# Kernel optimization log

Measured on AMD Instinct MI355X. Metric: run time of the kernel, lower is better.

The kernel has to match this reference:

```python
import jax, jax.numpy as jnp
import numpy as np

HIDDEN = 30

def setup_inputs() -> dict:
    key = jax.random.key(0)
    ks = jax.random.split(key, 12)
    N, E, F, G, C = 100000, 1600000, 128, 2048, 2
    x = jax.random.normal(ks[0], (N, F), dtype=jnp.float32)
    edge_index = jax.random.randint(ks[1], (2, E), 0, N, dtype=jnp.int64)
    batch = jnp.sort(jax.random.randint(ks[2], (N,), 0, G, dtype=jnp.int64))
    def glorot(k, shape):
        lim = np.sqrt(6.0 / (shape[0] + shape[1]))
        return jax.random.uniform(k, shape, jnp.float32, -lim, lim)
    return {
        'x': x, 'edge_index': edge_index, 'batch': batch, 'num_graphs': G,
        'W0': glorot(ks[3], (F, HIDDEN)), 'b0': jnp.zeros((HIDDEN,), jnp.float32),
        'W1': glorot(ks[4], (HIDDEN, HIDDEN)), 'b1': jnp.zeros((HIDDEN,), jnp.float32),
        'W2': glorot(ks[5], (HIDDEN, HIDDEN)), 'b2': jnp.zeros((HIDDEN,), jnp.float32),
        'W3': glorot(ks[6], (HIDDEN, HIDDEN)), 'b3': jnp.zeros((HIDDEN,), jnp.float32),
        'Wlin': glorot(ks[7], (4 * HIDDEN, C)), 'blin': jnp.zeros((C,), jnp.float32),
    }


def _gcn_norm(edge_index, num_nodes):
    # Add self-loops, compute symmetric normalization (PyG GCNConv default).
    loops = jnp.arange(num_nodes, dtype=edge_index.dtype)
    row = jnp.concatenate([edge_index[0], loops])
    col = jnp.concatenate([edge_index[1], loops])
    deg = jax.ops.segment_sum(jnp.ones_like(col, dtype=jnp.float32), col,
                              num_segments=num_nodes)
    dis = jnp.where(deg > 0, jax.lax.rsqrt(deg), 0.0)
    norm = dis[row] * dis[col]  # [E + N]
    return row, col, norm


def _gcn_conv(x, W, b, row, col, norm, num_nodes):
    xw = x @ W                              # [N, H] transform first
    msg = xw[row] * norm[:, None]           # gather + scale  [E+N, H]
    out = jax.ops.segment_sum(msg, col, num_segments=num_nodes)  # scatter-add
    return out + b


def _max_pool(x, batch, num_graphs):
    out = jax.ops.segment_max(x, batch, num_segments=num_graphs)
    return jnp.where(jnp.isneginf(out), 0.0, out)


def reference(x, edge_index, batch, num_graphs, W0, b0, W1, b1, W2, b2, W3, b3, Wlin, blin):
    N = x.shape[0]
    row, col, norm = _gcn_norm(edge_index, N)
    outs = []
    h = jax.nn.relu(_gcn_conv(x, W0, b0, row, col, norm, N))
    outs.append(_max_pool(h, batch, num_graphs))
    h = jax.nn.relu(_gcn_conv(h, W1, b1, row, col, norm, N))
    outs.append(_max_pool(h, batch, num_graphs))
    h = jax.nn.relu(_gcn_conv(h, W2, b2, row, col, norm, N))
    outs.append(_max_pool(h, batch, num_graphs))
    h = _gcn_conv(h, W3, b3, row, col, norm, N)  # no ReLU on last conv
    outs.append(_max_pool(h, batch, num_graphs))
    readout = jnp.concatenate(outs, axis=-1)     # [G, 4*HIDDEN]
    return readout @ Wlin + blin                 # [G, num_classes]
```

## Files before the change

### kernel.cpp

```cpp
#include <hip/hip_runtime.h>
#include <math.h>

#define HIDDEN 30
#define SP 32


__global__ void k_hist(const int* __restrict__ col, unsigned* __restrict__ deg, int E) {
    int e = blockIdx.x * blockDim.x + threadIdx.x;
    if (e < E) atomicAdd(&deg[col[e]], 1u);
}

__global__ void k_dis(const unsigned* __restrict__ deg, float* __restrict__ dis, int N) {
    int i = blockIdx.x * blockDim.x + threadIdx.x;
    if (i < N) dis[i] = rsqrtf((float)deg[i] + 1.0f);
}

__global__ void k_scan_block(const unsigned* __restrict__ deg, unsigned* __restrict__ inc,
                             unsigned* __restrict__ bsum, int N) {
    __shared__ unsigned s[1024];
    int i = blockIdx.x * 1024 + threadIdx.x;
    unsigned v = (i < N) ? deg[i] : 0u;
    s[threadIdx.x] = v;
    __syncthreads();
    for (int off = 1; off < 1024; off <<= 1) {
        unsigned t = (threadIdx.x >= off) ? s[threadIdx.x - off] : 0u;
        __syncthreads();
        s[threadIdx.x] += t;
        __syncthreads();
    }
    if (i < N) inc[i] = s[threadIdx.x];
    if (threadIdx.x == 1023) bsum[blockIdx.x] = s[1023];
}

__global__ void k_scan_bsums(unsigned* __restrict__ bsum, int nb) {
    __shared__ unsigned s[128];
    int i = threadIdx.x;
    s[i] = (i < nb) ? bsum[i] : 0u;
    __syncthreads();
    for (int off = 1; off < 128; off <<= 1) {
        unsigned t = (i >= off) ? s[i - off] : 0u;
        __syncthreads();
        s[i] += t;
        __syncthreads();
    }
    if (i < nb) bsum[i] = s[i];
}

__global__ void k_rowptr(const unsigned* __restrict__ bsum, unsigned* __restrict__ rowptr, int N) {
    int i = blockIdx.x * 1024 + threadIdx.x;
    if (i >= N) return;
    int blk = i >> 10;
    if (blk) rowptr[i + 1] += bsum[blk - 1];
    if (i == 0) rowptr[0] = 0u;
}

__global__ void k_cnt_copy(const unsigned* __restrict__ rowptr, unsigned* __restrict__ cnt, int N) {
    int i = blockIdx.x * blockDim.x + threadIdx.x;
    if (i < N) cnt[i] = rowptr[i];
}

__global__ void k_scatter(const int* __restrict__ row, const int* __restrict__ col,
                          unsigned* __restrict__ cnt, int* __restrict__ src, int E) {
    int e = blockIdx.x * blockDim.x + threadIdx.x;
    if (e >= E) return;
    int c = col[e];
    unsigned p = atomicAdd(&cnt[c], 1u);
    src[p] = row[e];
}

__global__ void k_gstart(const int* __restrict__ batch, int* __restrict__ gstart, int N, int G) {
    int i = blockIdx.x * blockDim.x + threadIdx.x;
    if (i >= N) return;
    int b = batch[i];
    if (i == 0) {
        for (int g = 0; g <= b; ++g) gstart[g] = 0;
    } else {
        int p = batch[i - 1];
        if (p != b) for (int g = p + 1; g <= b; ++g) gstart[g] = i;
    }
    if (i == N - 1) {
        for (int g = b + 1; g <= G; ++g) gstart[g] = N;
    }
}


__global__ void k_transform0(const float* __restrict__ x, const float* __restrict__ W,
                             const float* __restrict__ dis, float* __restrict__ S, int N) {
    __shared__ float Ws[128 * HIDDEN];
    __shared__ float Xs[8 * 128];
    for (int i = threadIdx.x; i < 128 * HIDDEN; i += 256) Ws[i] = W[i];
    int nb = blockIdx.x * 8;
    for (int i = threadIdx.x; i < 8 * 128; i += 256) {
        int nn = nb + (i >> 7);
        Xs[i] = (nn < N) ? x[(size_t)nn * 128 + (i & 127)] : 0.f;
    }
    __syncthreads();
    int nl = threadIdx.x >> 5, h = threadIdx.x & 31;
    int n = nb + nl;
    if (n >= N) return;
    float acc = 0.f;
    if (h < HIDDEN) {
        const float* xr = &Xs[nl * 128];
#pragma unroll 8
        for (int f = 0; f < 128; ++f) acc += xr[f] * Ws[f * HIDDEN + h];
        acc *= dis[n];
    }
    S[(size_t)n * SP + h] = (h < HIDDEN) ? acc : 0.f;
}

__global__ void k_transform_small(const float* __restrict__ in, const float* __restrict__ W,
                                  const float* __restrict__ dis, float* __restrict__ S, int N) {
    __shared__ float Ws[HIDDEN * HIDDEN];
    __shared__ float Bs[8 * SP];
    for (int i = threadIdx.x; i < HIDDEN * HIDDEN; i += 256) Ws[i] = W[i];
    int nb = blockIdx.x * 8;
    {
        int i = threadIdx.x;
        int nn = nb + (i >> 5);
        Bs[i] = (nn < N) ? in[(size_t)nn * SP + (i & 31)] : 0.f;
    }
    __syncthreads();
    int nl = threadIdx.x >> 5, h = threadIdx.x & 31;
    int n = nb + nl;
    if (n >= N) return;
    float acc = 0.f;
    if (h < HIDDEN) {
        const float* r = &Bs[nl * SP];
#pragma unroll
        for (int k = 0; k < HIDDEN; ++k) acc += r[k] * Ws[k * HIDDEN + h];
        acc *= dis[n];
    }
    S[(size_t)n * SP + h] = (h < HIDDEN) ? acc : 0.f;
}

__global__ void k_agg(const unsigned* __restrict__ rowptr, const int* __restrict__ src,
                      const float4* __restrict__ S4, const float* __restrict__ dis,
                      const float* __restrict__ b, float4* __restrict__ B4, int N, int do_relu) {
    int w = threadIdx.x >> 6;
    int lane = threadIdx.x & 63;
    int n = blockIdx.x * 4 + w;
    if (n >= N) return;
    int g = lane >> 3, s = lane & 7;
    float ax = 0.f, ay = 0.f, az = 0.f, aw = 0.f;
    if (g == 0) {
        float4 v = S4[(size_t)n * 8 + s];
        ax = v.x; ay = v.y; az = v.z; aw = v.w;
    }
    unsigned beg = rowptr[n], end = rowptr[n + 1];
    for (unsigned j = beg + g; j < end; j += 8) {
        int r = src[j];
        float4 v = S4[(size_t)r * 8 + s];
        ax += v.x; ay += v.y; az += v.z; aw += v.w;
    }
    for (int off = 8; off < 64; off <<= 1) {
        ax += __shfl_xor(ax, off);
        ay += __shfl_xor(ay, off);
        az += __shfl_xor(az, off);
        aw += __shfl_xor(aw, off);
    }
    if (g == 0) {
        float d = dis[n];
        int h = s * 4;
        float o0 = (h + 0 < HIDDEN) ? d * ax + b[h + 0] : 0.f;
        float o1 = (h + 1 < HIDDEN) ? d * ay + b[h + 1] : 0.f;
        float o2 = (h + 2 < HIDDEN) ? d * az + b[h + 2] : 0.f;
        float o3 = (h + 3 < HIDDEN) ? d * aw + b[h + 3] : 0.f;
        if (do_relu) {
            o0 = fmaxf(o0, 0.f); o1 = fmaxf(o1, 0.f);
            o2 = fmaxf(o2, 0.f); o3 = fmaxf(o3, 0.f);
        }
        B4[(size_t)n * 8 + s] = make_float4(o0, o1, o2, o3);
    }
}

__global__ void k_pool(const float* __restrict__ B, const int* __restrict__ gstart,
                       float* __restrict__ pooled, int G) {
    int g = blockIdx.x * 4 + (threadIdx.x >> 6);
    if (g >= G) return;
    int lane = threadIdx.x & 63;
    int h = lane & 31;
    int sub = lane >> 5;
    int beg = gstart[g], end = gstart[g + 1];
    float m = -INFINITY;
    if (h < HIDDEN) {
        for (int i = beg + sub; i < end; i += 2) m = fmaxf(m, B[(size_t)i * SP + h]);
    }
    float o = __shfl_down(m, 32);
    m = fmaxf(m, o);
    if (sub == 0 && h < HIDDEN) pooled[(size_t)g * HIDDEN + h] = (end > beg) ? m : 0.0f;
}

__global__ void k_final(const float* __restrict__ pooled, const float* __restrict__ Wlin,
                        const float* __restrict__ blin, float* __restrict__ out, int G) {
    int g = blockIdx.x * blockDim.x + threadIdx.x;
    if (g >= G) return;
    float a0 = blin[0], a1 = blin[1];
#pragma unroll
    for (int l = 0; l < 4; ++l) {
        for (int h = 0; h < HIDDEN; ++h) {
            float v = pooled[((size_t)l * G + g) * HIDDEN + h];
            int k = l * HIDDEN + h;
            a0 += v * Wlin[k * 2 + 0];
            a1 += v * Wlin[k * 2 + 1];
        }
    }
    out[g * 2 + 0] = a0;
    out[g * 2 + 1] = a1;
}

static inline size_t align256(size_t x) { return (x + 255) & ~(size_t)255; }

extern "C" void kernel_launch(void* const* d_in, const int* in_sizes, int n_in,
                              void* d_out, int out_size, void* d_ws, size_t ws_size,
                              hipStream_t stream) {
    const float* x     = (const float*)d_in[0];
    const int*   ei    = (const int*)d_in[1];
    const int*   batch = (const int*)d_in[2];
    const float* W0 = (const float*)d_in[4];
    const float* b0 = (const float*)d_in[5];
    const float* W1 = (const float*)d_in[6];
    const float* b1 = (const float*)d_in[7];
    const float* W2 = (const float*)d_in[8];
    const float* b2 = (const float*)d_in[9];
    const float* W3 = (const float*)d_in[10];
    const float* b3 = (const float*)d_in[11];
    const float* Wlin = (const float*)d_in[12];
    const float* blin = (const float*)d_in[13];

    const int N = in_sizes[0] / 128;
    const int E = in_sizes[1] / 2;
    const int G = out_size / 2;
    const int* row = ei;
    const int* col = ei + E;

    char* ws = (char*)d_ws;
    size_t off = 0;
    unsigned* deg    = (unsigned*)(ws + off); off += align256((size_t)N * 4);
    unsigned* cnt    = (unsigned*)(ws + off); off += align256((size_t)N * 4);
    unsigned* rowptr = (unsigned*)(ws + off); off += align256(((size_t)N + 1) * 4);
    unsigned* bsum   = (unsigned*)(ws + off); off += align256(128 * 4);
    int*      gstart = (int*)(ws + off);      off += align256(((size_t)G + 1) * 4);
    float*    dis    = (float*)(ws + off);    off += align256((size_t)N * 4);
    int*      src    = (int*)(ws + off);      off += align256((size_t)E * 4);
    float*    S      = (float*)(ws + off);    off += align256((size_t)N * SP * 4);
    float*    B      = (float*)(ws + off);    off += align256((size_t)N * SP * 4);
    float*    pooled = (float*)(ws + off);    off += align256((size_t)4 * G * HIDDEN * 4);

    const float* Wl[4] = {W0, W1, W2, W3};
    const float* bl[4] = {b0, b1, b2, b3};

    hipMemsetAsync(deg, 0, (size_t)N * 4, stream);
    k_hist<<<(E + 255) / 256, 256, 0, stream>>>(col, deg, E);
    k_dis<<<(N + 255) / 256, 256, 0, stream>>>(deg, dis, N);
    int nb = (N + 1023) / 1024;
    k_scan_block<<<nb, 1024, 0, stream>>>(deg, rowptr + 1, bsum, N);
    k_scan_bsums<<<1, 128, 0, stream>>>(bsum, nb);
    k_rowptr<<<nb, 1024, 0, stream>>>(bsum, rowptr, N);
    k_cnt_copy<<<(N + 255) / 256, 256, 0, stream>>>(rowptr, cnt, N);
    k_scatter<<<(E + 255) / 256, 256, 0, stream>>>(row, col, cnt, src, E);
    k_gstart<<<(N + 255) / 256, 256, 0, stream>>>(batch, gstart, N, G);

    int nblk8 = (N + 7) / 8;
    int nblk4 = (N + 3) / 4;
    for (int l = 0; l < 4; ++l) {
        if (l == 0) k_transform0<<<nblk8, 256, 0, stream>>>(x, W0, dis, S, N);
        else        k_transform_small<<<nblk8, 256, 0, stream>>>(B, Wl[l], dis, S, N);
        k_agg<<<nblk4, 256, 0, stream>>>(rowptr, src, (const float4*)S, dis, bl[l],
                                         (float4*)B, N, l < 3 ? 1 : 0);
        k_pool<<<(G + 3) / 4, 256, 0, stream>>>(B, gstart, pooled + (size_t)l * G * HIDDEN, G);
    }

    k_final<<<(G + 255) / 256, 256, 0, stream>>>(pooled, Wlin, blin, (float*)d_out, G);
}
```

Measured before the change: 652.3 us.

## Replace random CSR scatter with two-pass bucketed radix partition

The single-pass atomic scatter of edges into CSR order is replaced by a coarse partition. Edges are first bucketed by destination-node range using per-block shared histograms, a single-block scan, and a bucketed pair scatter. A per-bucket pass then does the fine atomic placement, so global atomics and writes stay within a localized node range for better cache locality. The cost is extra passes, an 8-byte pair buffer per edge, and a serial single-block scan over 256x256 entries.

```diff
diff --git a/kernel.cpp b/kernel.cpp
--- a/kernel.cpp
+++ b/kernel.cpp
@@ -14,6 +14,7 @@
     int i = blockIdx.x * blockDim.x + threadIdx.x;
     if (i < N) dis[i] = rsqrtf((float)deg[i] + 1.0f);
 }
+
 
 __global__ void k_scan_block(const unsigned* __restrict__ deg, unsigned* __restrict__ inc,
                              unsigned* __restrict__ bsum, int N) {
@@ -59,13 +60,73 @@
     if (i < N) cnt[i] = rowptr[i];
 }
 
-__global__ void k_scatter(const int* __restrict__ row, const int* __restrict__ col,
-                          unsigned* __restrict__ cnt, int* __restrict__ src, int E) {
-    int e = blockIdx.x * blockDim.x + threadIdx.x;
-    if (e >= E) return;
-    int c = col[e];
-    unsigned p = atomicAdd(&cnt[c], 1u);
-    src[p] = row[e];
+
+__global__ void k_bhist(const int* __restrict__ col, unsigned* __restrict__ blockhist,
+                        int E, int chunk, int nblocks, int shift, int NB) {
+    __shared__ unsigned h[256];
+    for (int i = threadIdx.x; i < NB; i += 256) h[i] = 0;
+    __syncthreads();
+    int s = blockIdx.x * chunk, e = min(E, s + chunk);
+    for (int j = s + threadIdx.x; j < e; j += 256) atomicAdd(&h[col[j] >> shift], 1u);
+    __syncthreads();
+    for (int i = threadIdx.x; i < NB; i += 256)
+        blockhist[(size_t)i * nblocks + blockIdx.x] = h[i];
+}
+
+__global__ void k_bscan(unsigned* __restrict__ a, int M) {
+    __shared__ unsigned s[1024];
+    __shared__ unsigned carry;
+    if (threadIdx.x == 0) carry = 0;
+    __syncthreads();
+    for (int base = 0; base < M; base += 1024) {
+        int i = base + threadIdx.x;
+        unsigned v = (i < M) ? a[i] : 0u;
+        s[threadIdx.x] = v;
+        __syncthreads();
+        for (int off = 1; off < 1024; off <<= 1) {
+            unsigned t = (threadIdx.x >= off) ? s[threadIdx.x - off] : 0u;
+            __syncthreads();
+            s[threadIdx.x] += t;
+            __syncthreads();
+        }
+        unsigned excl = s[threadIdx.x] - v + carry;
+        if (i < M) a[i] = excl;
+        __syncthreads();
+        if (threadIdx.x == 1023) carry += s[1023];
+        __syncthreads();
+    }
+}
+
+__global__ void k_bscatter(const int* __restrict__ row, const int* __restrict__ col,
+                           const unsigned* __restrict__ bh, int2* __restrict__ pairs,
+                           int E, int chunk, int nblocks, int shift, int NB) {
+    __shared__ unsigned base[256];
+    __shared__ unsigned cnt[256];
+    for (int i = threadIdx.x; i < NB; i += 256) {
+        base[i] = bh[(size_t)i * nblocks + blockIdx.x];
+        cnt[i] = 0;
+    }
+    __syncthreads();
+    int s = blockIdx.x * chunk, e = min(E, s + chunk);
+    for (int j = s + threadIdx.x; j < e; j += 256) {
+        int c = col[j];
+        int k = c >> shift;
+        unsigned off = base[k] + atomicAdd(&cnt[k], 1u);
+        pairs[off] = make_int2(row[j], c);
+    }
+}
+
+__global__ void k_fscatter(const unsigned* __restrict__ bh, const int2* __restrict__ pairs,
+                           unsigned* __restrict__ cnt, int* __restrict__ src,
+                           int E, int nblocks, int NB) {
+    int k = blockIdx.x;
+    unsigned s = bh[(size_t)k * nblocks];
+    unsigned e = (k + 1 < NB) ? bh[(size_t)(k + 1) * nblocks] : (unsigned)E;
+    for (unsigned j = s + threadIdx.x; j < e; j += blockDim.x) {
+        int2 p = pairs[j];
+        unsigned q = atomicAdd(&cnt[p.y], 1u);
+        src[q] = p.x;
+    }
 }
 
 __global__ void k_gstart(const int* __restrict__ batch, int* __restrict__ gstart, int N, int G) {
@@ -233,6 +294,13 @@
     const int* row = ei;
     const int* col = ei + E;
 
+    int shift = 9;
+    while (((N + (1 << shift) - 1) >> shift) > 256) shift++;
+    const int NB = (N + (1 << shift) - 1) >> shift;
+    const int nblocksA = 256;
+    const int chunk = (E + nblocksA - 1) / nblocksA;
+    const int M = NB * nblocksA;
+
     char* ws = (char*)d_ws;
     size_t off = 0;
     unsigned* deg    = (unsigned*)(ws + off); off += align256((size_t)N * 4);
@@ -241,6 +309,8 @@
     unsigned* bsum   = (unsigned*)(ws + off); off += align256(128 * 4);
     int*      gstart = (int*)(ws + off);      off += align256(((size_t)G + 1) * 4);
     float*    dis    = (float*)(ws + off);    off += align256((size_t)N * 4);
+    unsigned* bh     = (unsigned*)(ws + off); off += align256((size_t)M * 4);
+    int2*     pairs  = (int2*)(ws + off);     off += align256((size_t)E * 8);
     int*      src    = (int*)(ws + off);      off += align256((size_t)E * 4);
     float*    S      = (float*)(ws + off);    off += align256((size_t)N * SP * 4);
     float*    B      = (float*)(ws + off);    off += align256((size_t)N * SP * 4);
@@ -257,7 +327,10 @@
     k_scan_bsums<<<1, 128, 0, stream>>>(bsum, nb);
     k_rowptr<<<nb, 1024, 0, stream>>>(bsum, rowptr, N);
     k_cnt_copy<<<(N + 255) / 256, 256, 0, stream>>>(rowptr, cnt, N);
-    k_scatter<<<(E + 255) / 256, 256, 0, stream>>>(row, col, cnt, src, E);
+    k_bhist<<<nblocksA, 256, 0, stream>>>(col, bh, E, chunk, nblocksA, shift, NB);
+    k_bscan<<<1, 1024, 0, stream>>>(bh, M);
+    k_bscatter<<<nblocksA, 256, 0, stream>>>(row, col, bh, pairs, E, chunk, nblocksA, shift, NB);
+    k_fscatter<<<NB, 256, 0, stream>>>(bh, pairs, cnt, src, E, nblocksA, NB);
     k_gstart<<<(N + 255) / 256, 256, 0, stream>>>(batch, gstart, N, G);
 
     int nblk8 = (N + 7) / 8;
```

Result: slower. 670.8 us (+2.8%).
